# Optimization experiments

Hardware: AMD Instinct MI355X
Metric: run time of the kernel (lower is better)

Reference implementation:

```python
import jax, jax.numpy as jnp
import numpy as np

N_NODES = 50000
N_EDGES = 800000
IN_DIM = 128
HID_DIM = 128


def gcn_conv(x, edge_index, W, b):
    # PyG GCNConv: out = D^{-1/2} (A + I) D^{-1/2} X W + b
    n = x.shape[0]
    loop = jnp.arange(n)
    src = jnp.concatenate([edge_index[0], loop])
    dst = jnp.concatenate([edge_index[1], loop])
    deg = jax.ops.segment_sum(jnp.ones_like(dst, dtype=x.dtype), dst, num_segments=n)
    dinv = jax.lax.rsqrt(jnp.maximum(deg, 1.0))  # deg >= 1 with self-loops
    norm = dinv[src] * dinv[dst]                 # [E+N]
    h = x @ W                                    # [N, out_dim] dense transform first (smaller msgs)
    msg = h[src] * norm[:, None]                 # gather + scale
    return jax.ops.segment_sum(msg, dst, num_segments=n) + b  # scatter-add


def gcn_backbone(x, edge_index, W0, b0, W1, b1):
    h = jax.nn.relu(gcn_conv(x, edge_index, W0, b0))
    return gcn_conv(h, edge_index, W1, b1)


def setup_inputs() -> dict:
    key = jax.random.key(0)
    ks = jax.random.split(key, 8)
    s_in = 1.0 / np.sqrt(IN_DIM)
    s_h = 1.0 / np.sqrt(HID_DIM)
    return {
        "x1": jax.random.normal(ks[0], (N_NODES, IN_DIM), dtype=jnp.float32),
        "edge_index1": jax.random.randint(ks[1], (2, N_EDGES), 0, N_NODES, dtype=jnp.int32),
        "x2": jax.random.normal(ks[2], (N_NODES, IN_DIM), dtype=jnp.float32),
        "edge_index2": jax.random.randint(ks[3], (2, N_EDGES), 0, N_NODES, dtype=jnp.int32),
        "W0": jax.random.normal(ks[4], (IN_DIM, HID_DIM), dtype=jnp.float32) * s_in,
        "b0": jnp.zeros((HID_DIM,), dtype=jnp.float32),
        "W1": jax.random.normal(ks[5], (HID_DIM, HID_DIM), dtype=jnp.float32) * s_h,
        "b1": jnp.zeros((HID_DIM,), dtype=jnp.float32),
    }


def reference(x1, edge_index1, x2, edge_index2, W0, b0, W1, b1):
    z1 = gcn_backbone(x1, edge_index1, W0, b0, W1, b1)
    z2 = gcn_backbone(x2, edge_index2, W0, b0, W1, b1)
    return (z1, z2)
```

## Files before the change

### kernel.cpp

```cpp
#include <hip/hip_runtime.h>

#define GN 50000
#define GE 800000
#define GD 128
#define CAP 64
#define NBIN 8
#define BINW 6250
#define NCHUNK 400

typedef unsigned short u16;
typedef unsigned int u32;
typedef short bf16x8 __attribute__((ext_vector_type(8)));
typedef float f32x4 __attribute__((ext_vector_type(4)));
typedef u16 u16x8 __attribute__((ext_vector_type(8)));
typedef u16 u16x4 __attribute__((ext_vector_type(4)));

__device__ inline float bf2f_lo(u32 u) {
  union { u32 i; float f; } v; v.i = u << 16; return v.f;
}
__device__ inline float bf2f_hi(u32 u) {
  union { u32 i; float f; } v; v.i = u & 0xffff0000u; return v.f;
}
__device__ inline u16 f2bf(float f) {
  union { float f; u32 i; } v; v.f = f;
  u32 r = v.i + 0x7fffu + ((v.i >> 16) & 1u);
  return (u16)(r >> 16);
}
__device__ inline float rlf(float v, int l) {
  return __int_as_float(__builtin_amdgcn_readlane(__float_as_int(v), l));
}

#define NB ((GN + 63) / 64)
#define GEMM_BLKS (2 * NB)

#define FUSE_PER 200
#define FUSE_BLKS (FUSE_PER * 40)

__global__ __launch_bounds__(256) void k_prep(const float* __restrict__ W0,
                                              const float* __restrict__ W1,
                                              u16* __restrict__ Wf0,
                                              u16* __restrict__ Wf1,
                                              int* __restrict__ cnt) {
  int idx = blockIdx.x * 256 + threadIdx.x;
  if (idx < 4096) {
    const float* W = (idx & 2048) ? W1 : W0;
    u16* Wf = (idx & 2048) ? Wf1 : Wf0;
    int r = idx & 2047;
    int kq = r >> 9, cb = (r >> 6) & 7, lane = r & 63;
    int m16 = lane & 15, quad = lane >> 4;
    int k0 = kq * 32 + quad * 8;
    int n = cb * 16 + m16;
    u16x8 o;
#pragma unroll
    for (int j = 0; j < 8; j++) o[j] = f2bf(W[(k0 + j) * 128 + n]);
    *(u16x8*)&Wf[((kq * 8 + cb) * 64 + lane) * 8] = o;
  } else {
    int z = idx - 4096;
    if (z < 2 * GN) cnt[z] = 0;
  }
}

__global__ __launch_bounds__(256, 4) void k_fused1(const int* __restrict__ e1,
                                                   const int* __restrict__ e2,
                                                   int* __restrict__ cnt,
                                                   u16* __restrict__ bucket,
                                                   const float* __restrict__ X1,
                                                   const float* __restrict__ X2,
                                                   const u16* __restrict__ Wf,
                                                   u16* __restrict__ H) {
  __shared__ u16 Xs[64][136];

  int per = blockIdx.x / 40;
  int pos = blockIdx.x % 40;

  if (pos >= 8) {
    int bin = pos & 7;
    int seq = per * 4 + ((pos - 8) >> 3);
    int gb = seq >= NCHUNK;
    int chunk = seq - gb * NCHUNK;
    const int* E = gb ? e2 : e1;
    const int* src = E;
    const int* dst = E + GE;
    int* c = cnt + gb * GN;
    u16* bk = bucket + (size_t)gb * GN * CAP;

    int t0 = chunk * 256 + threadIdx.x;
    const int stride = NCHUNK * 256;
    int lo = bin * BINW, hi = lo + BINW;

    int s[8], d[8];
#pragma unroll
    for (int k = 0; k < 8; k++) {
      int e = t0 + k * stride;
      int ec = (e < GE) ? e : 0;
      s[k] = __builtin_nontemporal_load(&src[ec]);
      d[k] = __builtin_nontemporal_load(&dst[ec]);
      if (e >= GE) d[k] = -1;
    }
#pragma unroll
    for (int k = 0; k < 8; k++) {
      if (d[k] >= lo && d[k] < hi) {
        int slot = atomicAdd(&c[d[k]], 1);
        if (slot < CAP) bk[d[k] * CAP + slot] = (u16)s[k];
      }
    }
    return;
  }

  int g = per * 8 + pos;
  if (g >= GEMM_BLKS) return;
  int gb = g >= NB;
  int bid = g - gb * NB;
  const float* Xin = gb ? X2 : X1;
  u16* Hh = H + (size_t)gb * GN * GD;

  int t = threadIdx.x;
  int lane = t & 63, wave = t >> 6;
  int m16 = lane & 15, quad = lane >> 4;
  int r0 = bid * 64;

  bf16x8 bfr[4][2];
#pragma unroll
  for (int kq = 0; kq < 4; kq++)
#pragma unroll
    for (int c = 0; c < 2; c++)
      bfr[kq][c] = *(const bf16x8*)&Wf[((kq * 8 + wave * 2 + c) * 64 + lane) * 8];

  {
    const float4* Xv = (const float4*)Xin;
#pragma unroll
    for (int i = 0; i < 8; i++) {
      int idx = i * 256 + t;
      int row = idx >> 5, c4 = idx & 31;
      int gr = r0 + row; if (gr >= GN) gr = GN - 1;
      float4 v = Xv[(size_t)gr * 32 + c4];
      u16x4 u; u.x = f2bf(v.x); u.y = f2bf(v.y); u.z = f2bf(v.z); u.w = f2bf(v.w);
      *(u16x4*)&Xs[row][c4 * 4] = u;
    }
  }
  __syncthreads();

  f32x4 acc[4][2] = {};
#pragma unroll
  for (int kq = 0; kq < 4; kq++) {
#pragma unroll
    for (int rb = 0; rb < 4; rb++) {
      bf16x8 a = *(const bf16x8*)&Xs[rb * 16 + m16][kq * 32 + quad * 8];
      acc[rb][0] = __builtin_amdgcn_mfma_f32_16x16x32_bf16(a, bfr[kq][0], acc[rb][0], 0, 0, 0);
      acc[rb][1] = __builtin_amdgcn_mfma_f32_16x16x32_bf16(a, bfr[kq][1], acc[rb][1], 0, 0, 0);
    }
  }

#pragma unroll
  for (int rb = 0; rb < 4; rb++) {
#pragma unroll
    for (int i = 0; i < 4; i++) {
      int grow = r0 + rb * 16 + quad * 4 + i;
      if (grow < GN) {
#pragma unroll
        for (int c = 0; c < 2; c++)
          Hh[(size_t)grow * 128 + (wave * 2 + c) * 16 + m16] = f2bf(acc[rb][c][i]);
      }
    }
  }
}

__global__ __launch_bounds__(256, 4) void k_gemm2(const u16* __restrict__ X1,
                                                  const u16* __restrict__ X2,
                                                  const u16* __restrict__ Wf,
                                                  u16* __restrict__ H) {
  __shared__ u16 Xs[64][136];
  int gb = blockIdx.x >= NB;
  int bid = blockIdx.x - gb * NB;
  const u16* Xin = gb ? X2 : X1;
  u16* Hh = H + (size_t)gb * GN * GD;

  int t = threadIdx.x;
  int lane = t & 63, wave = t >> 6;
  int m16 = lane & 15, quad = lane >> 4;
  int r0 = bid * 64;

  bf16x8 bfr[4][2];
#pragma unroll
  for (int kq = 0; kq < 4; kq++)
#pragma unroll
    for (int c = 0; c < 2; c++)
      bfr[kq][c] = *(const bf16x8*)&Wf[((kq * 8 + wave * 2 + c) * 64 + lane) * 8];

  {
    const u16x8* Xv = (const u16x8*)Xin;
#pragma unroll
    for (int i = 0; i < 4; i++) {
      int idx = i * 256 + t;
      int row = idx >> 4, c8 = idx & 15;
      int gr = r0 + row; if (gr >= GN) gr = GN - 1;
      *(u16x8*)&Xs[row][c8 * 8] = Xv[(size_t)gr * 16 + c8];
    }
  }
  __syncthreads();

  f32x4 acc[4][2] = {};
#pragma unroll
  for (int kq = 0; kq < 4; kq++) {
#pragma unroll
    for (int rb = 0; rb < 4; rb++) {
      bf16x8 a = *(const bf16x8*)&Xs[rb * 16 + m16][kq * 32 + quad * 8];
      acc[rb][0] = __builtin_amdgcn_mfma_f32_16x16x32_bf16(a, bfr[kq][0], acc[rb][0], 0, 0, 0);
      acc[rb][1] = __builtin_amdgcn_mfma_f32_16x16x32_bf16(a, bfr[kq][1], acc[rb][1], 0, 0, 0);
    }
  }

#pragma unroll
  for (int rb = 0; rb < 4; rb++) {
#pragma unroll
    for (int i = 0; i < 4; i++) {
      int grow = r0 + rb * 16 + quad * 4 + i;
      if (grow < GN) {
#pragma unroll
        for (int c = 0; c < 2; c++)
          Hh[(size_t)grow * 128 + (wave * 2 + c) * 16 + m16] = f2bf(acc[rb][c][i]);
      }
    }
  }
}

template <bool FINAL>
__global__ __launch_bounds__(256) void k_agg(const u16* __restrict__ H,
                                             const u16* __restrict__ bucket,
                                             const int* __restrict__ cnt,
                                             const float* __restrict__ bias,
                                             void* __restrict__ out) {
  int widg = (blockIdx.x * 256 + threadIdx.x) >> 6;
  int lane = threadIdx.x & 63;
  if (widg >= 2 * GN) return;
  int gb = widg >= GN;
  int wid = widg - gb * GN;

  const int* c = cnt + gb * GN;
  const u16* bk = bucket + (size_t)gb * GN * CAP;
  const u32* Hv = (const u32*)H + (size_t)gb * GN * 64;

  int cw = c[wid];
  float dv = rsqrtf((float)(cw + 1));
  int deg = min(cw, CAP);

  int s_l = 0;
  float d_l = 0.f;
  if (lane < deg) {
    s_l = (int)bk[wid * CAP + lane];
    d_l = rsqrtf((float)(c[s_l] + 1));
  }

  u32 hs = Hv[(size_t)wid * 64 + lane];
  float ax = dv * bf2f_lo(hs);
  float ay = dv * bf2f_hi(hs);
  float2 bb = ((const float2*)bias)[lane];

  int dpad = (deg + 15) & ~15;
  for (int i = 0; i < dpad; i += 16) {
    int ss[16];
    u32 hh[16];
    float ww[16];
#pragma unroll
    for (int j = 0; j < 16; j++) ss[j] = __builtin_amdgcn_readlane(s_l, i + j);
#pragma unroll
    for (int j = 0; j < 16; j++) hh[j] = Hv[(size_t)ss[j] * 64 + lane];
#pragma unroll
    for (int j = 0; j < 16; j++) ww[j] = rlf(d_l, i + j);
#pragma unroll
    for (int j = 0; j < 16; j++) {
      ax += ww[j] * bf2f_lo(hh[j]);
      ay += ww[j] * bf2f_hi(hh[j]);
    }
  }

  float ox = dv * ax + bb.x;
  float oy = dv * ay + bb.y;
  if (!FINAL) {
    ox = fmaxf(ox, 0.f); oy = fmaxf(oy, 0.f);
    u32 packed = ((u32)f2bf(oy) << 16) | (u32)f2bf(ox);
    ((u32*)out)[(size_t)widg * 64 + lane] = packed;
  } else {
    ((float2*)out)[(size_t)widg * 64 + lane] = make_float2(ox, oy);
  }
}

extern "C" void kernel_launch(void* const* d_in, const int* in_sizes, int n_in,
                              void* d_out, int out_size, void* d_ws, size_t ws_size,
                              hipStream_t stream) {
  const float* x1 = (const float*)d_in[0];
  const int* ei1  = (const int*)d_in[1];
  const float* x2 = (const float*)d_in[2];
  const int* ei2  = (const int*)d_in[3];
  const float* W0 = (const float*)d_in[4];
  const float* b0 = (const float*)d_in[5];
  const float* W1 = (const float*)d_in[6];
  const float* b1 = (const float*)d_in[7];
  float* out = (float*)d_out;

  char* ws = (char*)d_ws;
  size_t off = 0;
  auto carve = [&](size_t bytes) -> char* {
    char* p = ws + off;
    off = (off + bytes + 511) & ~(size_t)511;
    return p;
  };
  int* cnt    = (int*)carve((size_t)2 * GN * 4);
  u16* bucket = (u16*)carve((size_t)2 * GN * CAP * 2);
  u16* h      = (u16*)carve((size_t)2 * GN * GD * 2);
  u16* a      = (u16*)carve((size_t)2 * GN * GD * 2);
  u16* W0f    = (u16*)carve((size_t)GD * GD * 2);
  u16* W1f    = (u16*)carve((size_t)GD * GD * 2);

  k_prep<<<(4096 + 2 * GN + 255) / 256, 256, 0, stream>>>(W0, W1, W0f, W1f, cnt);

  k_fused1<<<FUSE_BLKS, 256, 0, stream>>>(ei1, ei2, cnt, bucket,
                                          x1, x2, W0f, h);

  k_agg<false><<<(2 * GN * 64 + 255) / 256, 256, 0, stream>>>(h, bucket, cnt, b0, a);

  k_gemm2<<<2 * NB, 256, 0, stream>>>(a, a + (size_t)GN * GD, W1f, h);

  k_agg<true><<<(2 * GN * 64 + 255) / 256, 256, 0, stream>>>(h, bucket, cnt, b1, out);
}
```

Baseline: 311.4 us.

## Fuse first-layer aggregation with second GEMM into one kernel

Merges the layer-1 aggregation (gather, normalize, bias, ReLU) with the layer-2 dense transform. Each block aggregates 64 rows into shared memory and then runs MFMA on them, so the intermediate activation no longer makes a round trip through global memory and one launch is removed. The cost is less parallelism in the gather phase: each wave now handles 16 rows one after another instead of one row per wave across the whole grid. The launch-bounds occupancy hint for the first fused kernel is also raised from 4 to 8.

Result: slower. 333.6 us (+7.1%).

```diff
diff --git a/kernel.cpp b/kernel.cpp
--- a/kernel.cpp
+++ b/kernel.cpp
@@ -60,7 +60,7 @@
   }
 }
 
-__global__ __launch_bounds__(256, 4) void k_fused1(const int* __restrict__ e1,
+__global__ __launch_bounds__(256, 8) void k_fused1(const int* __restrict__ e1,
                                                    const int* __restrict__ e2,
                                                    int* __restrict__ cnt,
                                                    u16* __restrict__ bucket,
@@ -165,39 +165,80 @@
   }
 }
 
-__global__ __launch_bounds__(256, 4) void k_gemm2(const u16* __restrict__ X1,
-                                                  const u16* __restrict__ X2,
-                                                  const u16* __restrict__ Wf,
-                                                  u16* __restrict__ H) {
+__global__ __launch_bounds__(256) void k_aggemm(const u16* __restrict__ H,
+                                                const u16* __restrict__ bucket,
+                                                const int* __restrict__ cnt,
+                                                const float* __restrict__ bias,
+                                                const u16* __restrict__ Wf,
+                                                u16* __restrict__ H2) {
   __shared__ u16 Xs[64][136];
+
   int gb = blockIdx.x >= NB;
   int bid = blockIdx.x - gb * NB;
-  const u16* Xin = gb ? X2 : X1;
-  u16* Hh = H + (size_t)gb * GN * GD;
-
   int t = threadIdx.x;
   int lane = t & 63, wave = t >> 6;
+  int r0 = bid * 64;
+
+  const int* c = cnt + gb * GN;
+  const u16* bk = bucket + (size_t)gb * GN * CAP;
+  const u32* Hv = (const u32*)H + (size_t)gb * GN * 64;
+  u16* Hh = H2 + (size_t)gb * GN * GD;
+
+  float2 bb = ((const float2*)bias)[lane];
+
+  for (int it = 0; it < 16; ++it) {
+    int row = wave * 16 + it;
+    int wid = r0 + row;
+    u32 packed = 0;
+    if (wid < GN) {
+      int cw = c[wid];
+      float dv = rsqrtf((float)(cw + 1));
+      int deg = min(cw, CAP);
+
+      int s_l = 0;
+      float d_l = 0.f;
+      if (lane < deg) {
+        s_l = (int)bk[wid * CAP + lane];
+        d_l = rsqrtf((float)(c[s_l] + 1));
+      }
+
+      u32 hs = Hv[(size_t)wid * 64 + lane];
+      float ax = dv * bf2f_lo(hs);
+      float ay = dv * bf2f_hi(hs);
+
+      int dpad = (deg + 15) & ~15;
+      for (int i = 0; i < dpad; i += 16) {
+        int ss[16];
+        u32 hh[16];
+        float ww[16];
+#pragma unroll
+        for (int j = 0; j < 16; j++) ss[j] = __builtin_amdgcn_readlane(s_l, i + j);
+#pragma unroll
+        for (int j = 0; j < 16; j++) hh[j] = Hv[(size_t)ss[j] * 64 + lane];
+#pragma unroll
+        for (int j = 0; j < 16; j++) ww[j] = rlf(d_l, i + j);
+#pragma unroll
+        for (int j = 0; j < 16; j++) {
+          ax += ww[j] * bf2f_lo(hh[j]);
+          ay += ww[j] * bf2f_hi(hh[j]);
+        }
+      }
+
+      float ox = fmaxf(dv * ax + bb.x, 0.f);
+      float oy = fmaxf(dv * ay + bb.y, 0.f);
+      packed = ((u32)f2bf(oy) << 16) | (u32)f2bf(ox);
+    }
+    *(u32*)&Xs[row][lane * 2] = packed;
+  }
+  __syncthreads();
+
   int m16 = lane & 15, quad = lane >> 4;
-  int r0 = bid * 64;
-
   bf16x8 bfr[4][2];
 #pragma unroll
   for (int kq = 0; kq < 4; kq++)
 #pragma unroll
-    for (int c = 0; c < 2; c++)
-      bfr[kq][c] = *(const bf16x8*)&Wf[((kq * 8 + wave * 2 + c) * 64 + lane) * 8];
-
-  {
-    const u16x8* Xv = (const u16x8*)Xin;
-#pragma unroll
-    for (int i = 0; i < 4; i++) {
-      int idx = i * 256 + t;
-      int row = idx >> 4, c8 = idx & 15;
-      int gr = r0 + row; if (gr >= GN) gr = GN - 1;
-      *(u16x8*)&Xs[row][c8 * 8] = Xv[(size_t)gr * 16 + c8];
-    }
-  }
-  __syncthreads();
+    for (int cc = 0; cc < 2; cc++)
+      bfr[kq][cc] = *(const bf16x8*)&Wf[((kq * 8 + wave * 2 + cc) * 64 + lane) * 8];
 
   f32x4 acc[4][2] = {};
 #pragma unroll
@@ -217,19 +258,18 @@
       int grow = r0 + rb * 16 + quad * 4 + i;
       if (grow < GN) {
 #pragma unroll
-        for (int c = 0; c < 2; c++)
-          Hh[(size_t)grow * 128 + (wave * 2 + c) * 16 + m16] = f2bf(acc[rb][c][i]);
-      }
-    }
-  }
-}
-
-template <bool FINAL>
-__global__ __launch_bounds__(256) void k_agg(const u16* __restrict__ H,
-                                             const u16* __restrict__ bucket,
-                                             const int* __restrict__ cnt,
-                                             const float* __restrict__ bias,
-                                             void* __restrict__ out) {
+        for (int cc = 0; cc < 2; cc++)
+          Hh[(size_t)grow * 128 + (wave * 2 + cc) * 16 + m16] = f2bf(acc[rb][cc][i]);
+      }
+    }
+  }
+}
+
+__global__ __launch_bounds__(256) void k_aggF(const u16* __restrict__ H,
+                                              const u16* __restrict__ bucket,
+                                              const int* __restrict__ cnt,
+                                              const float* __restrict__ bias,
+                                              float* __restrict__ out) {
   int widg = (blockIdx.x * 256 + threadIdx.x) >> 6;
   int lane = threadIdx.x & 63;
   if (widg >= 2 * GN) return;
@@ -276,13 +316,7 @@
 
   float ox = dv * ax + bb.x;
   float oy = dv * ay + bb.y;
-  if (!FINAL) {
-    ox = fmaxf(ox, 0.f); oy = fmaxf(oy, 0.f);
-    u32 packed = ((u32)f2bf(oy) << 16) | (u32)f2bf(ox);
-    ((u32*)out)[(size_t)widg * 64 + lane] = packed;
-  } else {
-    ((float2*)out)[(size_t)widg * 64 + lane] = make_float2(ox, oy);
-  }
+  ((float2*)out)[(size_t)widg * 64 + lane] = make_float2(ox, oy);
 }
 
 extern "C" void kernel_launch(void* const* d_in, const int* in_sizes, int n_in,
@@ -308,7 +342,7 @@
   int* cnt    = (int*)carve((size_t)2 * GN * 4);
   u16* bucket = (u16*)carve((size_t)2 * GN * CAP * 2);
   u16* h      = (u16*)carve((size_t)2 * GN * GD * 2);
-  u16* a      = (u16*)carve((size_t)2 * GN * GD * 2);
+  u16* h2     = (u16*)carve((size_t)2 * GN * GD * 2);
   u16* W0f    = (u16*)carve((size_t)GD * GD * 2);
   u16* W1f    = (u16*)carve((size_t)GD * GD * 2);
 
@@ -317,9 +351,7 @@
   k_fused1<<<FUSE_BLKS, 256, 0, stream>>>(ei1, ei2, cnt, bucket,
                                           x1, x2, W0f, h);
 
-  k_agg<false><<<(2 * GN * 64 + 255) / 256, 256, 0, stream>>>(h, bucket, cnt, b0, a);
-
-  k_gemm2<<<2 * NB, 256, 0, stream>>>(a, a + (size_t)GN * GD, W1f, h);
-
-  k_agg<true><<<(2 * GN * 64 + 255) / 256, 256, 0, stream>>>(h, bucket, cnt, b1, out);
-}
+  k_aggemm<<<2 * NB, 256, 0, stream>>>(h, bucket, cnt, b0, W1f, h2);
+
+  k_aggF<<<(2 * GN * 64 + 255) / 256, 256, 0, stream>>>(h2, bucket, cnt, b1, out);
+}
```

## Interleave per-graph aggregation with other graph's GEMM in mixed kernels

Applied to the files above, without the earlier changes.

Splits the two-graph pipeline per graph and launches mixed kernels where some blocks compute the second-layer GEMM tile for one graph while others aggregate the other graph. This aims to overlap the compute-bound GEMM with the latency-bound gather and to avoid the idle tail between separate launches. It also raises the occupancy hint of the fused first kernel. In exchange there are more launches, and the GEMM blocks (one per 17) may end up unevenly scheduled.

Measured after the change: 332.9 us. +6.9%, slower.

```diff
diff --git a/kernel.cpp b/kernel.cpp
--- a/kernel.cpp
+++ b/kernel.cpp
@@ -35,6 +35,9 @@
 
 #define FUSE_PER 200
 #define FUSE_BLKS (FUSE_PER * 40)
+
+#define MIXP 17
+#define MIX_BLKS (NB * MIXP)
 
 __global__ __launch_bounds__(256) void k_prep(const float* __restrict__ W0,
                                               const float* __restrict__ W1,
@@ -60,7 +63,7 @@
   }
 }
 
-__global__ __launch_bounds__(256, 4) void k_fused1(const int* __restrict__ e1,
+__global__ __launch_bounds__(256, 8) void k_fused1(const int* __restrict__ e1,
                                                    const int* __restrict__ e2,
                                                    int* __restrict__ cnt,
                                                    u16* __restrict__ bucket,
@@ -165,17 +168,62 @@
   }
 }
 
-__global__ __launch_bounds__(256, 4) void k_gemm2(const u16* __restrict__ X1,
-                                                  const u16* __restrict__ X2,
-                                                  const u16* __restrict__ Wf,
-                                                  u16* __restrict__ H) {
-  __shared__ u16 Xs[64][136];
-  int gb = blockIdx.x >= NB;
-  int bid = blockIdx.x - gb * NB;
-  const u16* Xin = gb ? X2 : X1;
-  u16* Hh = H + (size_t)gb * GN * GD;
-
-  int t = threadIdx.x;
+template <bool FINAL>
+__device__ __forceinline__ void agg_one(int wid, int lane,
+                                        const int* __restrict__ c,
+                                        const u16* __restrict__ bk,
+                                        const u32* __restrict__ Hv,
+                                        float2 bb,
+                                        void* __restrict__ outp) {
+  int cw = c[wid];
+  float dv = rsqrtf((float)(cw + 1));
+  int deg = min(cw, CAP);
+
+  int s_l = 0;
+  float d_l = 0.f;
+  if (lane < deg) {
+    s_l = (int)bk[wid * CAP + lane];
+    d_l = rsqrtf((float)(c[s_l] + 1));
+  }
+
+  u32 hs = Hv[(size_t)wid * 64 + lane];
+  float ax = dv * bf2f_lo(hs);
+  float ay = dv * bf2f_hi(hs);
+
+  int dpad = (deg + 15) & ~15;
+  for (int i = 0; i < dpad; i += 16) {
+    int ss[16];
+    u32 hh[16];
+    float ww[16];
+#pragma unroll
+    for (int j = 0; j < 16; j++) ss[j] = __builtin_amdgcn_readlane(s_l, i + j);
+#pragma unroll
+    for (int j = 0; j < 16; j++) hh[j] = Hv[(size_t)ss[j] * 64 + lane];
+#pragma unroll
+    for (int j = 0; j < 16; j++) ww[j] = rlf(d_l, i + j);
+#pragma unroll
+    for (int j = 0; j < 16; j++) {
+      ax += ww[j] * bf2f_lo(hh[j]);
+      ay += ww[j] * bf2f_hi(hh[j]);
+    }
+  }
+
+  float ox = dv * ax + bb.x;
+  float oy = dv * ay + bb.y;
+  if (!FINAL) {
+    ox = fmaxf(ox, 0.f); oy = fmaxf(oy, 0.f);
+    u32 packed = ((u32)f2bf(oy) << 16) | (u32)f2bf(ox);
+    ((u32*)outp)[(size_t)wid * 64 + lane] = packed;
+  } else {
+    ((float2*)outp)[(size_t)wid * 64 + lane] = make_float2(ox, oy);
+  }
+}
+
+__device__ __forceinline__ void gemm_tile_bf16(int bid, int t,
+                                               const u16* __restrict__ Xin,
+                                               const u16* __restrict__ Wf,
+                                               u16* __restrict__ Hh,
+                                               u16 (*Xs)[136]) {
   int lane = t & 63, wave = t >> 6;
   int m16 = lane & 15, quad = lane >> 4;
   int r0 = bid * 64;
@@ -225,64 +273,43 @@
 }
 
 template <bool FINAL>
-__global__ __launch_bounds__(256) void k_agg(const u16* __restrict__ H,
-                                             const u16* __restrict__ bucket,
-                                             const int* __restrict__ cnt,
-                                             const float* __restrict__ bias,
-                                             void* __restrict__ out) {
-  int widg = (blockIdx.x * 256 + threadIdx.x) >> 6;
+__global__ __launch_bounds__(256) void k_agg_s(const u16* __restrict__ H,
+                                               const u16* __restrict__ bk,
+                                               const int* __restrict__ c,
+                                               const float* __restrict__ bias,
+                                               void* __restrict__ outp) {
+  int wid = blockIdx.x * 4 + (threadIdx.x >> 6);
   int lane = threadIdx.x & 63;
-  if (widg >= 2 * GN) return;
-  int gb = widg >= GN;
-  int wid = widg - gb * GN;
-
-  const int* c = cnt + gb * GN;
-  const u16* bk = bucket + (size_t)gb * GN * CAP;
-  const u32* Hv = (const u32*)H + (size_t)gb * GN * 64;
-
-  int cw = c[wid];
-  float dv = rsqrtf((float)(cw + 1));
-  int deg = min(cw, CAP);
-
-  int s_l = 0;
-  float d_l = 0.f;
-  if (lane < deg) {
-    s_l = (int)bk[wid * CAP + lane];
-    d_l = rsqrtf((float)(c[s_l] + 1));
-  }
-
-  u32 hs = Hv[(size_t)wid * 64 + lane];
-  float ax = dv * bf2f_lo(hs);
-  float ay = dv * bf2f_hi(hs);
+  if (wid >= GN) return;
   float2 bb = ((const float2*)bias)[lane];
-
-  int dpad = (deg + 15) & ~15;
-  for (int i = 0; i < dpad; i += 16) {
-    int ss[16];
-    u32 hh[16];
-    float ww[16];
-#pragma unroll
-    for (int j = 0; j < 16; j++) ss[j] = __builtin_amdgcn_readlane(s_l, i + j);
-#pragma unroll
-    for (int j = 0; j < 16; j++) hh[j] = Hv[(size_t)ss[j] * 64 + lane];
-#pragma unroll
-    for (int j = 0; j < 16; j++) ww[j] = rlf(d_l, i + j);
-#pragma unroll
-    for (int j = 0; j < 16; j++) {
-      ax += ww[j] * bf2f_lo(hh[j]);
-      ay += ww[j] * bf2f_hi(hh[j]);
-    }
-  }
-
-  float ox = dv * ax + bb.x;
-  float oy = dv * ay + bb.y;
-  if (!FINAL) {
-    ox = fmaxf(ox, 0.f); oy = fmaxf(oy, 0.f);
-    u32 packed = ((u32)f2bf(oy) << 16) | (u32)f2bf(ox);
-    ((u32*)out)[(size_t)widg * 64 + lane] = packed;
-  } else {
-    ((float2*)out)[(size_t)widg * 64 + lane] = make_float2(ox, oy);
-  }
+  agg_one<FINAL>(wid, lane, c, bk, (const u32*)H, bb, outp);
+}
+
+template <bool FINAL_AGG>
+__global__ __launch_bounds__(256) void k_mix(const u16* __restrict__ aggH,
+                                             const u16* __restrict__ aggBk,
+                                             const int* __restrict__ aggC,
+                                             const float* __restrict__ aggBias,
+                                             void* __restrict__ aggOut,
+                                             const u16* __restrict__ gX,
+                                             const u16* __restrict__ gWf,
+                                             u16* __restrict__ gH2) {
+  __shared__ u16 Xs[64][136];
+  int per = blockIdx.x / MIXP;
+  int pos = blockIdx.x % MIXP;
+  int t = threadIdx.x;
+
+  if (pos == 0) {
+    gemm_tile_bf16(per, t, gX, gWf, gH2, Xs);
+    return;
+  }
+
+  int ab = per * 16 + (pos - 1);
+  if (ab >= 12500) return;
+  int wid = ab * 4 + (t >> 6);
+  int lane = t & 63;
+  float2 bb = ((const float2*)aggBias)[lane];
+  agg_one<FINAL_AGG>(wid, lane, aggC, aggBk, (const u32*)aggH, bb, aggOut);
 }
 
 extern "C" void kernel_launch(void* const* d_in, const int* in_sizes, int n_in,
@@ -312,14 +339,25 @@
   u16* W0f    = (u16*)carve((size_t)GD * GD * 2);
   u16* W1f    = (u16*)carve((size_t)GD * GD * 2);
 
+  const size_t NGD = (size_t)GN * GD;
+  u16* h_g1 = h;            u16* h_g2 = h + NGD;
+  u16* a_g1 = a;            u16* a_g2 = a + NGD;
+  u16* h2_g1 = h_g1;        u16* h2_g2 = h_g2;
+  u16* bk_g1 = bucket;      u16* bk_g2 = bucket + (size_t)GN * CAP;
+  int* c_g1 = cnt;          int* c_g2 = cnt + GN;
+  float* out_g1 = out;      float* out_g2 = out + NGD;
+
   k_prep<<<(4096 + 2 * GN + 255) / 256, 256, 0, stream>>>(W0, W1, W0f, W1f, cnt);
 
-  k_fused1<<<FUSE_BLKS, 256, 0, stream>>>(ei1, ei2, cnt, bucket,
-                                          x1, x2, W0f, h);
-
-  k_agg<false><<<(2 * GN * 64 + 255) / 256, 256, 0, stream>>>(h, bucket, cnt, b0, a);
-
-  k_gemm2<<<2 * NB, 256, 0, stream>>>(a, a + (size_t)GN * GD, W1f, h);
-
-  k_agg<true><<<(2 * GN * 64 + 255) / 256, 256, 0, stream>>>(h, bucket, cnt, b1, out);
-}
+  k_fused1<<<FUSE_BLKS, 256, 0, stream>>>(ei1, ei2, cnt, bucket, x1, x2, W0f, h);
+
+  k_agg_s<false><<<12500, 256, 0, stream>>>(h_g1, bk_g1, c_g1, b0, a_g1);
+
+  k_mix<false><<<MIX_BLKS, 256, 0, stream>>>(h_g2, bk_g2, c_g2, b0, a_g2,
+                                             a_g1, W1f, h2_g1);
+
+  k_mix<true><<<MIX_BLKS, 256, 0, stream>>>(h2_g1, bk_g1, c_g1, b1, out_g1,
+                                            a_g2, W1f, h2_g2);
+
+  k_agg_s<true><<<12500, 256, 0, stream>>>(h2_g2, bk_g2, c_g2, b1, out_g2);
+}
```
